# Optimization experiments

Measured on AMD Instinct MI355X. Metric: run time of the kernel, lower is better.

Reference implementation:

```python
import jax, jax.numpy as jnp
import numpy as np

EPS = 1e-12  # matches torch F.normalize eps

def _l2norm(v, axis):
    n = jnp.sqrt(jnp.sum(v * v, axis=axis, keepdims=True))
    return v / jnp.maximum(n, EPS)

def setup_inputs() -> dict:
    key = jax.random.key(0)
    k1, k2, k3 = jax.random.split(key, 3)
    N, D, H, W, K = 64, 128, 56, 56, 64
    x = jax.random.normal(k1, (N, D, H, W), dtype=jnp.float32)
    conv_w = jax.random.normal(k2, (K, D), dtype=jnp.float32) * 0.05
    centroids = jax.random.uniform(k3, (K, D), dtype=jnp.float32)
    return {"x": x, "conv_w": conv_w, "centroids": centroids}

def reference(x, conv_w, centroids):
    # x: [N, D, H, W]; conv_w: [K, D] (1x1 conv, no bias); centroids: [K, D]
    N, D, H, W = x.shape
    K = centroids.shape[0]
    L = H * W
    # descriptor-wise L2 normalization over channel dim
    x = _l2norm(x, axis=1)
    xf = x.reshape(N, D, L)                      # [N, D, L]
    # 1x1 conv == per-pixel matmul; softmax over clusters
    logits = jnp.einsum('ndl,kd->nkl', xf, conv_w)  # [N, K, L]
    a = jax.nn.softmax(logits, axis=1)              # [N, K, L]
    # vlad[n,k,d] = sum_l a[n,k,l] * (x[n,d,l] - c[k,d])
    #            = (a @ x^T) - (sum_l a) * c   (matmul reformulation)
    vlad = jnp.einsum('nkl,ndl->nkd', a, xf) - a.sum(axis=-1)[:, :, None] * centroids[None]
    # intra-normalize over descriptor dim, flatten, global L2 normalize
    vlad = _l2norm(vlad, axis=2)
    vlad = vlad.reshape(N, K * D)
    vlad = _l2norm(vlad, axis=1)
    return vlad
```

## Files before the change

### kernel.cpp

```cpp
#include <hip/hip_runtime.h>

#define N_   64
#define D_   128
#define L_   3136
#define K_   64
#define TL_  64
#define NG_  8
#define ASH  72

typedef short  short8  __attribute__((ext_vector_type(8)));
typedef short  short4v __attribute__((ext_vector_type(4)));
typedef float  f32x16  __attribute__((ext_vector_type(16)));

static __device__ __forceinline__ unsigned short f2bf(float f) {
    unsigned u = __float_as_uint(f);
    return (unsigned short)((u + 0x7FFFu + ((u >> 16) & 1u)) >> 16);
}
static __device__ __forceinline__ float bf2f(short s) {
    return __uint_as_float(((unsigned)(unsigned short)s) << 16);
}

#define BARX() asm volatile("s_waitcnt lgkmcnt(0)\n\ts_barrier" ::: "memory")

__global__ __launch_bounds__(256, 2)
void vlad_main(const float* __restrict__ x, const float* __restrict__ w,
               float* __restrict__ vout, float* __restrict__ aout,
               int vstride, int astride)
{
    __shared__ __align__(16) short L1[TL_ * D_];
    __shared__ __align__(16) short L2[D_ * TL_];
    __shared__ __align__(16) char  AsRaw[K_ * ASH * 2];
    __shared__ float nrm_lds[TL_];
    __shared__ float dred[4][32];

    const int t    = threadIdx.x;
    const int lane = t & 63;
    const int wv   = __builtin_amdgcn_readfirstlane(t >> 6);
    const int n    = blockIdx.x / NG_;
    const int g    = blockIdx.x % NG_;
    const int tile0 = (g == 0) ? 0 : (7 + 6 * (g - 1));
    const int ntile = (g == 0) ? 7 : 6;

    const int Mt = wv & 1;
    const int lg = lane >> 5;
    const int lm = lane & 31;

    char* L1b = (char*)L1;
    char* L2b = (char*)L2;
    short* AsS = (short*)AsRaw;
    float (*red_ss)[68] = (float (*)[68])AsRaw;

    short8 wf[8];
#pragma unroll
    for (int ks = 0; ks < 8; ++ks) {
        const float* wp = w + (size_t)(32 * Mt + lm) * D_ + 16 * ks + 8 * lg;
        const float4 wa = *(const float4*)wp;
        const float4 wb = *(const float4*)(wp + 4);
        short8 f;
        f[0]=f2bf(wa.x); f[1]=f2bf(wa.y); f[2]=f2bf(wa.z); f[3]=f2bf(wa.w);
        f[4]=f2bf(wb.x); f[5]=f2bf(wb.y); f[6]=f2bf(wb.z); f[7]=f2bf(wb.w);
        wf[ks] = f;
    }

    f32x16 acc0 = {0};
    f32x16 acc1 = {0};
    float asum_acc = 0.f;

    const int q  = t >> 4;
    const int l0 = (t & 15) * 4;
    const float* xb = x + (size_t)n * D_ * L_;

    float4 v[8];
    {
        const int p0 = tile0 * TL_;
#pragma unroll
        for (int r = 0; r < 8; ++r)
            v[r] = *(const float4*)(xb + (size_t)(8 * q + r) * L_ + p0 + l0);
    }

    for (int ti = 0; ti < ntile; ++ti) {
#pragma unroll
        for (int j = 0; j < 4; ++j) {
            float s = 0.f;
#pragma unroll
            for (int r = 0; r < 8; ++r) {
                const float val = (&v[r].x)[j];
                s = fmaf(val, val, s);
            }
            red_ss[q][l0 + j] = s;
        }
        unsigned short sh[8][4];
#pragma unroll
        for (int r = 0; r < 8; ++r)
#pragma unroll
            for (int j = 0; j < 4; ++j) sh[r][j] = f2bf((&v[r].x)[j]);
#pragma unroll
        for (int j = 0; j < 4; ++j) {
            const int l = l0 + j;
            short8 f;
#pragma unroll
            for (int r = 0; r < 8; ++r) f[r] = sh[r][j];
            *(short8*)(L1b + l * 256 + ((16 * q) ^ ((l & 15) << 4))) = f;
        }
#pragma unroll
        for (int r = 0; r < 8; ++r) {
            const int d = 8 * q + r;
            short4v f;
#pragma unroll
            for (int j = 0; j < 4; ++j) f[j] = sh[r][j];
            *(short4v*)(L2b + d * 128 + ((l0 * 2) ^ ((d & 7) << 4))) = f;
        }
        if (ti + 1 < ntile) {
            const int p0n = (tile0 + ti + 1) * TL_;
#pragma unroll
            for (int r = 0; r < 8; ++r)
                v[r] = *(const float4*)(xb + (size_t)(8 * q + r) * L_ + p0n + l0);
        }
        BARX();
        if (t < TL_) {
            float ss = 0.f;
#pragma unroll
            for (int qq = 0; qq < 16; ++qq) ss += red_ss[qq][t];
            nrm_lds[t] = fmaxf(sqrtf(ss), 1e-12f);
        }
        f32x16 r1 = {0};
        {
            const int l = 32 * (wv >> 1) + lm;
            const int rowoff = l * 256;
            const int swz = (l & 15) << 4;
            __builtin_amdgcn_s_setprio(1);
#pragma unroll
            for (int ks = 0; ks < 8; ++ks) {
                const short8 bfr = *(short8*)(L1b + rowoff + (((16 * ks + 8 * lg) * 2) ^ swz));
                r1 = __builtin_amdgcn_mfma_f32_32x32x16_bf16(wf[ks], bfr, r1, 0, 0, 0);
            }
            __builtin_amdgcn_s_setprio(0);
        }
        const int myl = 32 * (wv >> 1) + lm;
        float ss16 = 0.f;
#pragma unroll
        for (int qq = 0; qq < 16; ++qq) ss16 += red_ss[qq][myl];
        const float invp = 1.f / fmaxf(sqrtf(ss16), 1e-12f);
        float e[16];
        float s = 0.f;
#pragma unroll
        for (int r = 0; r < 16; ++r) { e[r] = __expf(r1[r] * invp); s += e[r]; }
        s += __shfl_xor(s, 32);
        if (lane < 32) dred[wv][lm] = s;
        BARX();
        const float denom = dred[wv][lm] + dred[wv ^ 1][lm];
        const float sc = invp / denom;
        {
            const int colp = 32 * (wv >> 1) + lm;
#pragma unroll
            for (int r = 0; r < 16; ++r) {
                const int k = 32 * Mt + (r & 3) + 8 * (r >> 2) + 4 * lg;
                AsS[k * ASH + colp] = (short)f2bf(e[r] * sc);
            }
        }
        BARX();
        {
            short8 af[4];
            const char* arow = AsRaw + (size_t)(32 * Mt + lm) * (ASH * 2);
#pragma unroll
            for (int ks = 0; ks < 4; ++ks)
                af[ks] = *(const short8*)(arow + (16 * ks + 8 * lg) * 2);
            __builtin_amdgcn_s_setprio(1);
#pragma unroll
            for (int nt = 0; nt < 2; ++nt) {
                const int dk = 32 * (2 * (wv >> 1) + nt) + lm;
                const int rowoff = dk * 128;
                const int swz = (dk & 7) << 4;
                f32x16 a = (nt == 0) ? acc0 : acc1;
#pragma unroll
                for (int ks = 0; ks < 4; ++ks) {
                    const short8 bfr = *(short8*)(L2b + rowoff + (((16 * ks + 8 * lg) * 2) ^ swz));
                    a = __builtin_amdgcn_mfma_f32_32x32x16_bf16(af[ks], bfr, a, 0, 0, 0);
                }
                if (nt == 0) acc0 = a; else acc1 = a;
            }
            __builtin_amdgcn_s_setprio(0);
        }
        {
            const int k  = 16 * wv + (lane & 15);
            const int c4 = lane >> 4;
            const char* ap = AsRaw + (size_t)k * (ASH * 2) + c4 * 32;
            const short8 a0 = *(const short8*)ap;
            const short8 a1 = *(const short8*)(ap + 16);
            float ps = 0.f;
#pragma unroll
            for (int i = 0; i < 8; ++i) {
                ps = fmaf(bf2f(a0[i]), nrm_lds[16 * c4 + i],     ps);
                ps = fmaf(bf2f(a1[i]), nrm_lds[16 * c4 + 8 + i], ps);
            }
            ps += __shfl_xor(ps, 16);
            ps += __shfl_xor(ps, 32);
            asum_acc += ps;
        }
        BARX();
    }
    {
        const int dbase0 = 32 * (2 * (wv >> 1));
        float* vb = vstride ? (vout + (size_t)g * vstride) : vout;
#pragma unroll
        for (int r = 0; r < 16; ++r) {
            const int k = 32 * Mt + (r & 3) + 8 * (r >> 2) + 4 * lg;
            float* row = vb + ((size_t)n * K_ + k) * D_ + lm;
            if (vstride) {
                row[dbase0]      = acc0[r];
                row[dbase0 + 32] = acc1[r];
            } else {
                atomicAdd(&row[dbase0],      acc0[r]);
                atomicAdd(&row[dbase0 + 32], acc1[r]);
            }
        }
        if (lane < 16) {
            const int k = 16 * wv + lane;
            if (astride) aout[(size_t)g * astride + n * K_ + k] = asum_acc;
            else atomicAdd(&aout[n * K_ + k], asum_acc);
        }
    }
}

__global__ __launch_bounds__(256)
void vlad_fin(const float* __restrict__ vacc, const float* __restrict__ asum,
              const float* __restrict__ cent, float* __restrict__ out, int npart)
{
    const int t   = threadIdx.x;
    const int b   = blockIdx.x;
    const int n   = b >> 3;
    const int oct = b & 7;
    const int k   = oct * 8 + (t >> 5);
    const int c   = t & 31;

    float a = 0.f;
#pragma unroll 4
    for (int g = 0; g < npart; ++g) a += asum[(size_t)g * (N_ * K_) + n * K_ + k];

    const size_t off4 = ((size_t)(n * K_ + k) * D_ >> 2) + c;
    float4 v = make_float4(0.f, 0.f, 0.f, 0.f);
#pragma unroll 4
    for (int g = 0; g < npart; ++g) {
        const float4 s = ((const float4*)vacc)[(size_t)g * ((size_t)N_ * K_ * D_ >> 2) + off4];
        v.x += s.x; v.y += s.y; v.z += s.z; v.w += s.w;
    }
    const float4 cc = ((const float4*)cent)[((size_t)k * D_ >> 2) + c];
    v.x -= a * cc.x; v.y -= a * cc.y; v.z -= a * cc.z; v.w -= a * cc.w;
    float ss = v.x * v.x + v.y * v.y + v.z * v.z + v.w * v.w;
    ss += __shfl_xor(ss, 1);
    ss += __shfl_xor(ss, 2);
    ss += __shfl_xor(ss, 4);
    ss += __shfl_xor(ss, 8);
    ss += __shfl_xor(ss, 16);
    const float s1 = 0.125f / fmaxf(sqrtf(ss), 1e-12f);
    float4 o;
    o.x = v.x * s1; o.y = v.y * s1; o.z = v.z * s1; o.w = v.w * s1;
    ((float4*)out)[off4] = o;
}

extern "C" void kernel_launch(void* const* d_in, const int* in_sizes, int n_in,
                              void* d_out, int out_size, void* d_ws, size_t ws_size,
                              hipStream_t stream)
{
    const float* x = (const float*)d_in[0];
    const float* w = (const float*)d_in[1];
    const float* c = (const float*)d_in[2];
    float* out = (float*)d_out;

    const size_t vs  = (size_t)N_ * K_ * D_;
    const size_t as_ = (size_t)N_ * K_;
    const size_t need = (NG_ * vs + NG_ * as_) * sizeof(float);
    float* vacc = (float*)d_ws;

    if (ws_size >= need) {
        float* ap = vacc + NG_ * vs;
        vlad_main<<<dim3(N_ * NG_), dim3(256), 0, stream>>>(x, w, vacc, ap,
                                                            (int)vs, (int)as_);
        vlad_fin<<<dim3(N_ * 8), dim3(256), 0, stream>>>(vacc, ap, c, out, NG_);
    } else {
        float* ap = vacc + vs;
        hipMemsetAsync(d_ws, 0, (vs + as_) * sizeof(float), stream);
        vlad_main<<<dim3(N_ * NG_), dim3(256), 0, stream>>>(x, w, vacc, ap, 0, 0);
        vlad_fin<<<dim3(N_ * 8), dim3(256), 0, stream>>>(vacc, ap, c, out, 1);
    }
}
```

Baseline: 37.87 us.

## Split pixel tiles across 12 blocks per image and use packed bf16 conversion

Raises the number of blocks per image from 8 to 12, so each block handles 4 or 5 pixel tiles instead of 6 or 7. This gives more blocks for occupancy across CUs, at the cost of more partial results to reduce downstream. It also replaces scalar manual float-to-bf16 rounding with packed __float22bfloat162_rn conversions, which cuts ALU work and register shuffling in the tile staging loop. The reduction stage not shown must agree with the new group count.

After: 42.47 us. +12.1%, slower.

```diff
diff --git a/kernel.cpp b/kernel.cpp
--- a/kernel.cpp
+++ b/kernel.cpp
@@ -1,11 +1,12 @@
 #include <hip/hip_runtime.h>
+#include <hip/hip_bf16.h>
 
 #define N_   64
 #define D_   128
 #define L_   3136
 #define K_   64
 #define TL_  64
-#define NG_  8
+#define NG_  12
 #define ASH  72
 
 typedef short  short8  __attribute__((ext_vector_type(8)));
@@ -18,6 +19,10 @@
 }
 static __device__ __forceinline__ float bf2f(short s) {
     return __uint_as_float(((unsigned)(unsigned short)s) << 16);
+}
+static __device__ __forceinline__ unsigned pk2(float lo, float hi) {
+    __hip_bfloat162 b = __float22bfloat162_rn(make_float2(lo, hi));
+    return *reinterpret_cast<unsigned*>(&b);
 }
 
 #define BARX() asm volatile("s_waitcnt lgkmcnt(0)\n\ts_barrier" ::: "memory")
@@ -38,8 +43,8 @@
     const int wv   = __builtin_amdgcn_readfirstlane(t >> 6);
     const int n    = blockIdx.x / NG_;
     const int g    = blockIdx.x % NG_;
-    const int tile0 = (g == 0) ? 0 : (7 + 6 * (g - 1));
-    const int ntile = (g == 0) ? 7 : 6;
+    const int tile0 = (g == 0) ? 0 : (4 * g + 1);
+    const int ntile = (g == 0) ? 5 : 4;
 
     const int Mt = wv & 1;
     const int lg = lane >> 5;
@@ -56,10 +61,10 @@
         const float* wp = w + (size_t)(32 * Mt + lm) * D_ + 16 * ks + 8 * lg;
         const float4 wa = *(const float4*)wp;
         const float4 wb = *(const float4*)(wp + 4);
-        short8 f;
-        f[0]=f2bf(wa.x); f[1]=f2bf(wa.y); f[2]=f2bf(wa.z); f[3]=f2bf(wa.w);
-        f[4]=f2bf(wb.x); f[5]=f2bf(wb.y); f[6]=f2bf(wb.z); f[7]=f2bf(wb.w);
-        wf[ks] = f;
+        union { unsigned u[4]; short8 s; } f;
+        f.u[0] = pk2(wa.x, wa.y); f.u[1] = pk2(wa.z, wa.w);
+        f.u[2] = pk2(wb.x, wb.y); f.u[3] = pk2(wb.z, wb.w);
+        wf[ks] = f.s;
     }
 
     f32x16 acc0 = {0};
@@ -89,26 +94,23 @@
             }
             red_ss[q][l0 + j] = s;
         }
-        unsigned short sh[8][4];
-#pragma unroll
-        for (int r = 0; r < 8; ++r)
-#pragma unroll
-            for (int j = 0; j < 4; ++j) sh[r][j] = f2bf((&v[r].x)[j]);
 #pragma unroll
         for (int j = 0; j < 4; ++j) {
             const int l = l0 + j;
-            short8 f;
-#pragma unroll
-            for (int r = 0; r < 8; ++r) f[r] = sh[r][j];
-            *(short8*)(L1b + l * 256 + ((16 * q) ^ ((l & 15) << 4))) = f;
+            union { unsigned u[4]; short8 s; } f;
+            f.u[0] = pk2((&v[0].x)[j], (&v[1].x)[j]);
+            f.u[1] = pk2((&v[2].x)[j], (&v[3].x)[j]);
+            f.u[2] = pk2((&v[4].x)[j], (&v[5].x)[j]);
+            f.u[3] = pk2((&v[6].x)[j], (&v[7].x)[j]);
+            *(short8*)(L1b + l * 256 + ((16 * q) ^ ((l & 15) << 4))) = f.s;
         }
 #pragma unroll
         for (int r = 0; r < 8; ++r) {
             const int d = 8 * q + r;
-            short4v f;
-#pragma unroll
-            for (int j = 0; j < 4; ++j) f[j] = sh[r][j];
-            *(short4v*)(L2b + d * 128 + ((l0 * 2) ^ ((d & 7) << 4))) = f;
+            union { unsigned u[2]; short4v s; } f;
+            f.u[0] = pk2(v[r].x, v[r].y);
+            f.u[1] = pk2(v[r].z, v[r].w);
+            *(short4v*)(L2b + d * 128 + ((l0 * 2) ^ ((d & 7) << 4))) = f.s;
         }
         if (ti + 1 < ntile) {
             const int p0n = (tile0 + ti + 1) * TL_;
```
